# Kernel optimization log

Hardware: AMD Instinct MI355X
Metric: run time of the kernel (lower is better)

## Reference

```python
import jax, jax.numpy as jnp
import numpy as np
from jax import lax

CR = 16        # opt.cr (temporal dim)
HEADS = 4      # num_heads
DIM = 64       # dim == channel count c
B = 2          # true batch; input batch = B*CR
H = W = 128


def setup_inputs() -> dict:
    key = jax.random.key(0)
    k1, k2, k3, k4 = jax.random.split(key, 4)
    return {
        "x": jax.random.normal(k1, (B * CR, DIM, H, W), jnp.float32),
        "ln_weight": jnp.ones((DIM,), jnp.float32),
        "ln_bias": jnp.zeros((DIM,), jnp.float32),
        "qkv_w": jax.random.normal(k2, (3 * CR, CR), jnp.float32) * 0.05,   # 1x1 conv
        "dw_w": jax.random.normal(k3, (3 * CR, 1, 3, 3), jnp.float32) * 0.1,  # depthwise 3x3
        "proj_w": jax.random.normal(k4, (DIM, DIM), jnp.float32) * 0.05,   # 1x1 conv
        "temperature": jnp.ones((HEADS, 1, 1), jnp.float32),
    }


def reference(x, ln_weight, ln_bias, qkv_w, dw_w, proj_w, temperature):
    b, c, h, w = x.shape
    Bt = b // CR
    # WithBias LayerNorm over channel dim (per spatial location), eps=1e-5
    mu = jnp.mean(x, axis=1, keepdims=True)
    var = jnp.mean(jnp.square(x - mu), axis=1, keepdims=True)
    xn = (x - mu) / jnp.sqrt(var + 1e-5)
    xn = xn * ln_weight[None, :, None, None] + ln_bias[None, :, None, None]
    # (B*cr, c, h, w) -> (B, cr, c, h, w) -> (B*c, cr, h, w)
    x_in = xn.reshape(Bt, CR, c, h, w).transpose(0, 2, 1, 3, 4).reshape(Bt * c, CR, h, w)
    # 1x1 qkv conv (no bias)
    qkv = jnp.einsum('oc,bchw->bohw', qkv_w, x_in)
    # depthwise 3x3 conv, padding 1
    qkv = lax.conv_general_dilated(qkv, dw_w, (1, 1), 'SAME',
                                   feature_group_count=3 * CR,
                                   dimension_numbers=('NCHW', 'OIHW', 'NCHW'))
    q, k, v = jnp.split(qkv, 3, axis=1)
    ch = CR // HEADS  # per-head channel dim

    def heads(t):
        return t.reshape(Bt * c, HEADS, ch, h * w)

    def l2n(t):
        n = jnp.sqrt(jnp.sum(jnp.square(t), axis=-1, keepdims=True))
        return t / jnp.maximum(n, 1e-12)

    q, k, v = heads(q), heads(k), heads(v)
    q, k = l2n(q), l2n(k)
    # transposed (channel) attention: small ch x ch scores
    attn = jnp.einsum('bhcn,bhdn->bhcd', q, k) * temperature[None]
    attn = jax.nn.softmax(attn, axis=-1)
    out = jnp.einsum('bhcd,bhdn->bhcn', attn, v)  # (B*c, heads, ch, hw)
    # (B*c, cr, h, w) -> (B, c, cr, h, w) -> (B*cr, c, h, w)
    out = out.reshape(Bt * c, CR, h, w).reshape(Bt, c, CR, h, w)
    out = out.transpose(0, 2, 1, 3, 4).reshape(b, c, h, w)
    # 1x1 project_out
    return jnp.einsum('oc,bchw->bohw', proj_w, out)
```

## Files before the change

kernel.cpp:

```cpp
#include <hip/hip_runtime.h>
#include <hip/hip_fp16.h>

__device__ __forceinline__ float2 h2f2(unsigned int u) {
  return __half22float2(__builtin_bit_cast(__half2, u));
}
__device__ __forceinline__ unsigned int f2h2(float a, float b) {
  return __builtin_bit_cast(unsigned int, __floats2half2_rn(a, b));
}

#if __has_builtin(__builtin_amdgcn_fdot2)
typedef _Float16 h2v __attribute__((ext_vector_type(2)));
__device__ __forceinline__ float fdot2(unsigned int a, unsigned int b, float c) {
  return __builtin_amdgcn_fdot2(__builtin_bit_cast(h2v, a),
                                __builtin_bit_cast(h2v, b), c, false);
}
#else
__device__ __forceinline__ float fdot2(unsigned int a, unsigned int b, float c) {
  float2 fa = h2f2(a), fb = h2f2(b);
  return fmaf(fa.y, fb.y, fmaf(fa.x, fb.x, c));
}
#endif

__global__ __launch_bounds__(256) void k_stats(const float2* __restrict__ x2,
                                               float4* __restrict__ stats4) {
  int id = blockIdx.x * 256 + threadIdx.x;
  int bb = id >> 13;
  int jp = id & 8191;
  const float2* xp = x2 + ((size_t)bb << 19) + jp;
  float s0 = 0.f, q0 = 0.f, s1 = 0.f, q1 = 0.f;
#pragma unroll
  for (int ci = 0; ci < 64; ++ci) {
    float2 v = xp[(size_t)ci << 13];
    s0 += v.x; q0 = fmaf(v.x, v.x, q0);
    s1 += v.y; q1 = fmaf(v.y, v.y, q1);
  }
  float mu0 = s0 * (1.f / 64.f), mu1 = s1 * (1.f / 64.f);
  float4 r;
  r.x = mu0; r.y = rsqrtf(fmaf(-mu0, mu0, q0 * (1.f / 64.f)) + 1e-5f);
  r.z = mu1; r.w = rsqrtf(fmaf(-mu1, mu1, q1 * (1.f / 64.f)) + 1e-5f);
  stats4[id] = r;
}

__global__ __launch_bounds__(256) void k_wpack(
    const float* __restrict__ qkvw, const float* __restrict__ dww,
    const float* __restrict__ projw, unsigned int* __restrict__ qkvpk,
    unsigned int* __restrict__ dwpk, unsigned int* __restrict__ projpk) {
  int t = blockIdx.x * 256 + threadIdx.x;
  if (t < 2048) {
    int o = t >> 5, c2 = t & 31;
    projpk[t] = f2h2(projw[(o << 6) + 2 * c2], projw[(o << 6) + 2 * c2 + 1]);
  } else if (t < 2432) {
    int i = t - 2048;
    int ch = i >> 3, tp = i & 7;
    qkvpk[i] = f2h2(qkvw[(ch << 4) + 2 * tp], qkvw[(ch << 4) + 2 * tp + 1]);
  } else if (t < 2648) {
    int i = t - 2432;
    int pl = i / 9, k = i - pl * 9;
    dwpk[i] = f2h2(dww[18 * pl + k], dww[18 * pl + 9 + k]);
  }
}

__global__ __launch_bounds__(256) void k_fused(
    const float* __restrict__ x, const float2* __restrict__ stats2,
    const float* __restrict__ lnw, const float* __restrict__ lnb,
    const unsigned int* __restrict__ qkvpk, const unsigned int* __restrict__ dwpk,
    unsigned int* __restrict__ vbuf, float* __restrict__ Sacc,
    float* __restrict__ Nacc) {
  __shared__ unsigned int pre[2520];
  int tid = threadIdx.x;
  int bc = blockIdx.y, bt = bc >> 6, ci = bc & 63;
  int tx0 = (blockIdx.x & 3) << 5, ty0 = (blockIdx.x >> 2) << 4;
  float lw = lnw[ci], lb = lnb[ci];

  unsigned int wc[3][8];
  int waddr[3];
  {
    size_t xci = ((size_t)(bt * 1024 + ci)) << 14;
    int sbase = bt << 18;
#pragma unroll
    for (int it = 0; it < 3; ++it) {
      int pos = tid + (it << 8);
      bool act = pos < 612;
      int hy = pos / 34, hx = pos - hy * 34;
      int gy = ty0 + hy - 1, gx = tx0 + hx - 1;
      bool ok = act && ((unsigned)gy < 128u) && ((unsigned)gx < 128u);
      waddr[it] = act ? (hy * 35 + hx) : -1;
      int gp = (gy << 7) + gx;
#pragma unroll
      for (int tp = 0; tp < 8; ++tp) {
        unsigned int w = 0;
        if (ok) {
          float x0 = x[xci + ((size_t)(2 * tp) << 20) + gp];
          float x1 = x[xci + ((size_t)(2 * tp + 1) << 20) + gp];
          float2 s0 = stats2[sbase + (2 * tp) * 16384 + gp];
          float2 s1 = stats2[sbase + (2 * tp + 1) * 16384 + gp];
          w = f2h2(fmaf((x0 - s0.x) * s0.y, lw, lb),
                   fmaf((x1 - s1.x) * s1.y, lw, lb));
        }
        wc[it][tp] = w;
      }
    }
  }

  int iy = tid >> 4, jx = tid & 15;
  int dwbase = iy * 35 + 2 * jx;

  for (int h = 0; h < 4; ++h) {
#pragma unroll
    for (int it = 0; it < 3; ++it) {
      if (waddr[it] >= 0) {
        float acc[8];
#pragma unroll
        for (int c = 0; c < 8; ++c) {
          int gch = (c < 4) ? (4 * h + c) : (16 + 4 * h + (c - 4));
          float s = 0.f;
#pragma unroll
          for (int tp = 0; tp < 8; ++tp)
            s = fdot2(wc[it][tp], qkvpk[gch * 8 + tp], s);
          acc[c] = s;
        }
#pragma unroll
        for (int pl = 0; pl < 4; ++pl)
          pre[pl * 630 + waddr[it]] = f2h2(acc[2 * pl], acc[2 * pl + 1]);
      }
    }
    __syncthreads();
    unsigned int qkw[8];
#pragma unroll
    for (int pl = 0; pl < 4; ++pl) {
      int gpl = (pl < 2) ? (2 * h + pl) : (8 + 2 * h + (pl - 2));
      const unsigned int* wp = dwpk + gpl * 9;
      __half2 a0 = __floats2half2_rn(0.f, 0.f), a1 = a0;
      int base = pl * 630 + dwbase;
#pragma unroll
      for (int dy = 0; dy < 3; ++dy) {
        __half2 d0 = __builtin_bit_cast(__half2, pre[base + dy * 35 + 0]);
        __half2 d1 = __builtin_bit_cast(__half2, pre[base + dy * 35 + 1]);
        __half2 d2 = __builtin_bit_cast(__half2, pre[base + dy * 35 + 2]);
        __half2 d3 = __builtin_bit_cast(__half2, pre[base + dy * 35 + 3]);
        __half2 w0 = __builtin_bit_cast(__half2, wp[dy * 3 + 0]);
        __half2 w1 = __builtin_bit_cast(__half2, wp[dy * 3 + 1]);
        __half2 w2 = __builtin_bit_cast(__half2, wp[dy * 3 + 2]);
        a0 = __hfma2(w0, d0, a0); a0 = __hfma2(w1, d1, a0); a0 = __hfma2(w2, d2, a0);
        a1 = __hfma2(w0, d1, a1); a1 = __hfma2(w1, d2, a1); a1 = __hfma2(w2, d3, a1);
      }
      unsigned int u0 = __builtin_bit_cast(unsigned int, a0);
      unsigned int u1 = __builtin_bit_cast(unsigned int, a1);
      qkw[2 * pl]     = (u0 & 0xFFFFu) | (u1 << 16);
      qkw[2 * pl + 1] = (u0 >> 16) | (u1 & 0xFFFF0000u);
    }
    __syncthreads();
#pragma unroll
    for (int r = 0; r < 8; ++r) pre[r * 272 + tid] = qkw[r];
    __syncthreads();
    {
      int cd = tid >> 4, pc = tid & 15;
      int cc = cd >> 2, dd = cd & 3;
      const unsigned int* qrow = pre + cc * 272;
      const unsigned int* krow = pre + (4 + dd) * 272;
      float s = 0.f;
#pragma unroll
      for (int i = 0; i < 16; ++i)
        s = fdot2(qrow[pc + (i << 4)], krow[pc + (i << 4)], s);
      s += __shfl_xor(s, 1); s += __shfl_xor(s, 2);
      s += __shfl_xor(s, 4); s += __shfl_xor(s, 8);
      if (pc == 0) atomicAdd(&Sacc[((bc << 2) + h) * 16 + cc * 4 + dd], s);
    }
    {
      int row = tid >> 5, pc = tid & 31;
      const unsigned int* rp = pre + row * 272;
      float n = 0.f;
#pragma unroll
      for (int i = 0; i < 8; ++i) {
        unsigned int v = rp[pc + (i << 5)];
        n = fdot2(v, v, n);
      }
      n += __shfl_xor(n, 1); n += __shfl_xor(n, 2); n += __shfl_xor(n, 4);
      n += __shfl_xor(n, 8); n += __shfl_xor(n, 16);
      if (pc == 0) {
        int g = (row < 4) ? (4 * h + row) : (16 + 4 * h + (row - 4));
        atomicAdd(&Nacc[(bc << 5) + g], n);
      }
    }
    __syncthreads();
  }

  for (int vc = 0; vc < 2; ++vc) {
#pragma unroll
    for (int it = 0; it < 3; ++it) {
      if (waddr[it] >= 0) {
        float acc[8];
#pragma unroll
        for (int c = 0; c < 8; ++c) {
          int gch = 32 + 8 * vc + c;
          float s = 0.f;
#pragma unroll
          for (int tp = 0; tp < 8; ++tp)
            s = fdot2(wc[it][tp], qkvpk[gch * 8 + tp], s);
          acc[c] = s;
        }
#pragma unroll
        for (int pl = 0; pl < 4; ++pl)
          pre[pl * 630 + waddr[it]] = f2h2(acc[2 * pl], acc[2 * pl + 1]);
      }
    }
    __syncthreads();
#pragma unroll
    for (int pl = 0; pl < 4; ++pl) {
      int gpl = 16 + 4 * vc + pl;
      const unsigned int* wp = dwpk + gpl * 9;
      __half2 a0 = __floats2half2_rn(0.f, 0.f), a1 = a0;
      int base = pl * 630 + dwbase;
#pragma unroll
      for (int dy = 0; dy < 3; ++dy) {
        __half2 d0 = __builtin_bit_cast(__half2, pre[base + dy * 35 + 0]);
        __half2 d1 = __builtin_bit_cast(__half2, pre[base + dy * 35 + 1]);
        __half2 d2 = __builtin_bit_cast(__half2, pre[base + dy * 35 + 2]);
        __half2 d3 = __builtin_bit_cast(__half2, pre[base + dy * 35 + 3]);
        __half2 w0 = __builtin_bit_cast(__half2, wp[dy * 3 + 0]);
        __half2 w1 = __builtin_bit_cast(__half2, wp[dy * 3 + 1]);
        __half2 w2 = __builtin_bit_cast(__half2, wp[dy * 3 + 2]);
        a0 = __hfma2(w0, d0, a0); a0 = __hfma2(w1, d1, a0); a0 = __hfma2(w2, d2, a0);
        a1 = __hfma2(w0, d1, a1); a1 = __hfma2(w1, d2, a1); a1 = __hfma2(w2, d3, a1);
      }
      uint2 st2;
      st2.x = __builtin_bit_cast(unsigned int, a0);
      st2.y = __builtin_bit_cast(unsigned int, a1);
      size_t idx = ((size_t)(bc * 8 + 4 * vc + pl) << 14) +
                   (size_t)((ty0 + iy) << 7) + tx0 + 2 * jx;
      *reinterpret_cast<uint2*>(vbuf + idx) = st2;
    }
    __syncthreads();
  }
}

__global__ __launch_bounds__(256) void k_softmax(
    const float* __restrict__ Sacc, const float* __restrict__ Nacc,
    const float* __restrict__ temp, unsigned int* __restrict__ attnpk) {
  int idx = blockIdx.x * 256 + threadIdx.x;
  if (idx >= 512) return;
  int b = idx >> 2, hd = idx & 3;
  int bt = b >> 6, ci = b & 63;
  float tp = temp[hd];
  float iq[4], ik[4];
#pragma unroll
  for (int c = 0; c < 4; ++c) {
    iq[c] = 1.f / fmaxf(sqrtf(Nacc[(b << 5) + (hd << 2) + c]), 1e-12f);
    ik[c] = 1.f / fmaxf(sqrtf(Nacc[(b << 5) + 16 + (hd << 2) + c]), 1e-12f);
  }
  const float* Sp = Sacc + ((b << 2) + hd) * 16;
#pragma unroll
  for (int c = 0; c < 4; ++c) {
    float l[4];
#pragma unroll
    for (int d = 0; d < 4; ++d) l[d] = Sp[c * 4 + d] * iq[c] * ik[d] * tp;
    float m = fmaxf(fmaxf(l[0], l[1]), fmaxf(l[2], l[3]));
    float e0 = expf(l[0] - m), e1 = expf(l[1] - m);
    float e2 = expf(l[2] - m), e3 = expf(l[3] - m);
    float inv = 1.f / (e0 + e1 + e2 + e3);
    unsigned int* dst = attnpk + ((((bt * 4 + hd) * 4 + c) << 7) + ci * 2);
    dst[0] = f2h2(e0 * inv, e1 * inv);
    dst[1] = f2h2(e2 * inv, e3 * inv);
  }
}

__global__ __launch_bounds__(256) void k_outproj(
    const unsigned int* __restrict__ vbuf, const unsigned int* __restrict__ attnpk,
    const unsigned int* __restrict__ projpk, float* __restrict__ out) {
  int comb = blockIdx.y;
  int bt = comb >> 4, hd = (comb >> 2) & 3, c = comb & 3;
  int px = (blockIdx.x << 8) + threadIdx.x;

  const unsigned int* apk = attnpk + (((bt * 4 + hd) * 4 + c) << 7);
  float acc[64];
#pragma unroll
  for (int o = 0; o < 64; ++o) acc[o] = 0.f;

  size_t vbase = ((((size_t)bt * 512) + hd * 2) << 14) + px;
  for (int ci2 = 0; ci2 < 32; ++ci2) {
    size_t off0 = vbase + (((size_t)(2 * ci2) * 8) << 14);
    size_t off1 = off0 + ((size_t)8 << 14);
    unsigned int v0a = vbuf[off0];
    unsigned int v0b = vbuf[off0 + (1 << 14)];
    unsigned int v1a = vbuf[off1];
    unsigned int v1b = vbuf[off1 + (1 << 14)];
    float y0 = fdot2(v0a, apk[4 * ci2 + 0], fdot2(v0b, apk[4 * ci2 + 1], 0.f));
    float y1 = fdot2(v1a, apk[4 * ci2 + 2], fdot2(v1b, apk[4 * ci2 + 3], 0.f));
    unsigned int y2 = f2h2(y0, y1);
#pragma unroll
    for (int o = 0; o < 64; ++o)
      acc[o] = fdot2(y2, projpk[(o << 5) + ci2], acc[o]);
  }
  float* op = out + (((size_t)comb << 6) << 14) + px;
#pragma unroll
  for (int o = 0; o < 64; ++o) op[(size_t)o << 14] = acc[o];
}

extern "C" void kernel_launch(void* const* d_in, const int* in_sizes, int n_in,
                              void* d_out, int out_size, void* d_ws, size_t ws_size,
                              hipStream_t stream) {
  const float* x = (const float*)d_in[0];
  const float* lnw = (const float*)d_in[1];
  const float* lnb = (const float*)d_in[2];
  const float* qkvw = (const float*)d_in[3];
  const float* dww = (const float*)d_in[4];
  const float* projw = (const float*)d_in[5];
  const float* temp = (const float*)d_in[6];
  float* out = (float*)d_out;

  unsigned int* vbuf = (unsigned int*)d_ws;
  char* tail = (char*)d_ws + 67108864ull;
  float4* stats4 = (float4*)tail;
  float* Sacc = (float*)(tail + 4194304ull);
  float* Nacc = Sacc + 8192;
  unsigned int* attnpk = (unsigned int*)(Nacc + 4096);
  unsigned int* projpk = attnpk + 4096;
  unsigned int* qkvpk = projpk + 2048;
  unsigned int* dwpk = qkvpk + 384;

  hipMemsetAsync(Sacc, 0, (8192 + 4096) * sizeof(float), stream);
  k_stats<<<dim3(1024), dim3(256), 0, stream>>>((const float2*)x, stats4);
  k_wpack<<<dim3(11), dim3(256), 0, stream>>>(qkvw, dww, projw, qkvpk, dwpk, projpk);
  k_fused<<<dim3(32, 128), dim3(256), 0, stream>>>(
      x, (const float2*)stats4, lnw, lnb, qkvpk, dwpk, vbuf, Sacc, Nacc);
  k_softmax<<<dim3(2), dim3(256), 0, stream>>>(Sacc, Nacc, temp, attnpk);
  k_outproj<<<dim3(64, 32), dim3(256), 0, stream>>>(vbuf, attnpk, projpk, out);
}
```

Before: 207.2 us.

## Process two heads per pass in fused kernel and two pixels per thread in outproj

The fused kernel now handles two heads per iteration, and all eight V planes in one pass, using a doubled shared buffer. This halves the number of barrier-separated phases and atomic rounds. The output projection kernel now computes two adjacent pixels per thread with vectorized loads and stores, which reuses each projection weight load and halves the grid. The cost is more registers (128 accumulators in outproj, 16 packed values in fused) and double the LDS, which may reduce occupancy.

```diff
diff --git a/kernel.cpp b/kernel.cpp
--- a/kernel.cpp
+++ b/kernel.cpp
@@ -66,7 +66,7 @@
     const unsigned int* __restrict__ qkvpk, const unsigned int* __restrict__ dwpk,
     unsigned int* __restrict__ vbuf, float* __restrict__ Sacc,
     float* __restrict__ Nacc) {
-  __shared__ unsigned int pre[2520];
+  __shared__ unsigned int pre[5040];
   int tid = threadIdx.x;
   int bc = blockIdx.y, bt = bc >> 6, ci = bc & 63;
   int tx0 = (blockIdx.x & 3) << 5, ty0 = (blockIdx.x >> 2) << 4;
@@ -105,30 +105,29 @@
   int iy = tid >> 4, jx = tid & 15;
   int dwbase = iy * 35 + 2 * jx;
 
-  for (int h = 0; h < 4; ++h) {
+  for (int m = 0; m < 2; ++m) {
 #pragma unroll
     for (int it = 0; it < 3; ++it) {
       if (waddr[it] >= 0) {
-        float acc[8];
-#pragma unroll
-        for (int c = 0; c < 8; ++c) {
-          int gch = (c < 4) ? (4 * h + c) : (16 + 4 * h + (c - 4));
-          float s = 0.f;
-#pragma unroll
-          for (int tp = 0; tp < 8; ++tp)
-            s = fdot2(wc[it][tp], qkvpk[gch * 8 + tp], s);
-          acc[c] = s;
+#pragma unroll
+        for (int pl = 0; pl < 8; ++pl) {
+          int cE = 2 * pl;
+          int gchE = (cE < 8) ? (8 * m + cE) : (16 + 8 * m + (cE - 8));
+          float sE = 0.f, sO = 0.f;
+#pragma unroll
+          for (int tp = 0; tp < 8; ++tp) {
+            sE = fdot2(wc[it][tp], qkvpk[gchE * 8 + tp], sE);
+            sO = fdot2(wc[it][tp], qkvpk[(gchE + 1) * 8 + tp], sO);
+          }
+          pre[pl * 630 + waddr[it]] = f2h2(sE, sO);
         }
-#pragma unroll
-        for (int pl = 0; pl < 4; ++pl)
-          pre[pl * 630 + waddr[it]] = f2h2(acc[2 * pl], acc[2 * pl + 1]);
       }
     }
     __syncthreads();
-    unsigned int qkw[8];
-#pragma unroll
-    for (int pl = 0; pl < 4; ++pl) {
-      int gpl = (pl < 2) ? (2 * h + pl) : (8 + 2 * h + (pl - 2));
+    unsigned int qkw[16];
+#pragma unroll
+    for (int pl = 0; pl < 8; ++pl) {
+      int gpl = (pl < 4) ? (4 * m + pl) : (8 + 4 * m + (pl - 4));
       const unsigned int* wp = dwpk + gpl * 9;
       __half2 a0 = __floats2half2_rn(0.f, 0.f), a1 = a0;
       int base = pl * 630 + dwbase;
@@ -151,86 +150,80 @@
     }
     __syncthreads();
 #pragma unroll
-    for (int r = 0; r < 8; ++r) pre[r * 272 + tid] = qkw[r];
+    for (int r = 0; r < 16; ++r) pre[r * 272 + tid] = qkw[r];
     __syncthreads();
     {
-      int cd = tid >> 4, pc = tid & 15;
-      int cc = cd >> 2, dd = cd & 3;
-      const unsigned int* qrow = pre + cc * 272;
-      const unsigned int* krow = pre + (4 + dd) * 272;
+      int combo = tid >> 3, pc = tid & 7;
+      int hp = combo >> 4, cd = combo & 15, cc = cd >> 2, dd = cd & 3;
+      const unsigned int* qrow = pre + (4 * hp + cc) * 272;
+      const unsigned int* krow = pre + (8 + 4 * hp + dd) * 272;
       float s = 0.f;
 #pragma unroll
-      for (int i = 0; i < 16; ++i)
-        s = fdot2(qrow[pc + (i << 4)], krow[pc + (i << 4)], s);
-      s += __shfl_xor(s, 1); s += __shfl_xor(s, 2);
-      s += __shfl_xor(s, 4); s += __shfl_xor(s, 8);
-      if (pc == 0) atomicAdd(&Sacc[((bc << 2) + h) * 16 + cc * 4 + dd], s);
+      for (int i = 0; i < 32; ++i)
+        s = fdot2(qrow[pc + (i << 3)], krow[pc + (i << 3)], s);
+      s += __shfl_xor(s, 1); s += __shfl_xor(s, 2); s += __shfl_xor(s, 4);
+      if (pc == 0)
+        atomicAdd(&Sacc[((bc << 2) + 2 * m + hp) * 16 + cc * 4 + dd], s);
     }
     {
-      int row = tid >> 5, pc = tid & 31;
+      int row = tid >> 4, pc = tid & 15;
       const unsigned int* rp = pre + row * 272;
       float n = 0.f;
 #pragma unroll
-      for (int i = 0; i < 8; ++i) {
-        unsigned int v = rp[pc + (i << 5)];
+      for (int i = 0; i < 16; ++i) {
+        unsigned int v = rp[pc + (i << 4)];
         n = fdot2(v, v, n);
       }
-      n += __shfl_xor(n, 1); n += __shfl_xor(n, 2); n += __shfl_xor(n, 4);
-      n += __shfl_xor(n, 8); n += __shfl_xor(n, 16);
+      n += __shfl_xor(n, 1); n += __shfl_xor(n, 2);
+      n += __shfl_xor(n, 4); n += __shfl_xor(n, 8);
       if (pc == 0) {
-        int g = (row < 4) ? (4 * h + row) : (16 + 4 * h + (row - 4));
+        int g = (row < 8) ? (8 * m + row) : (16 + 8 * m + (row - 8));
         atomicAdd(&Nacc[(bc << 5) + g], n);
       }
     }
     __syncthreads();
   }
 
-  for (int vc = 0; vc < 2; ++vc) {
-#pragma unroll
-    for (int it = 0; it < 3; ++it) {
-      if (waddr[it] >= 0) {
-        float acc[8];
-#pragma unroll
-        for (int c = 0; c < 8; ++c) {
-          int gch = 32 + 8 * vc + c;
-          float s = 0.f;
-#pragma unroll
-          for (int tp = 0; tp < 8; ++tp)
-            s = fdot2(wc[it][tp], qkvpk[gch * 8 + tp], s);
-          acc[c] = s;
+#pragma unroll
+  for (int it = 0; it < 3; ++it) {
+    if (waddr[it] >= 0) {
+#pragma unroll
+      for (int pl = 0; pl < 8; ++pl) {
+        int gchE = 32 + 2 * pl;
+        float sE = 0.f, sO = 0.f;
+#pragma unroll
+        for (int tp = 0; tp < 8; ++tp) {
+          sE = fdot2(wc[it][tp], qkvpk[gchE * 8 + tp], sE);
+          sO = fdot2(wc[it][tp], qkvpk[(gchE + 1) * 8 + tp], sO);
         }
-#pragma unroll
-        for (int pl = 0; pl < 4; ++pl)
-          pre[pl * 630 + waddr[it]] = f2h2(acc[2 * pl], acc[2 * pl + 1]);
-      }
-    }
-    __syncthreads();
-#pragma unroll
-    for (int pl = 0; pl < 4; ++pl) {
-      int gpl = 16 + 4 * vc + pl;
-      const unsigned int* wp = dwpk + gpl * 9;
-      __half2 a0 = __floats2half2_rn(0.f, 0.f), a1 = a0;
-      int base = pl * 630 + dwbase;
-#pragma unroll
-      for (int dy = 0; dy < 3; ++dy) {
-        __half2 d0 = __builtin_bit_cast(__half2, pre[base + dy * 35 + 0]);
-        __half2 d1 = __builtin_bit_cast(__half2, pre[base + dy * 35 + 1]);
-        __half2 d2 = __builtin_bit_cast(__half2, pre[base + dy * 35 + 2]);
-        __half2 d3 = __builtin_bit_cast(__half2, pre[base + dy * 35 + 3]);
-        __half2 w0 = __builtin_bit_cast(__half2, wp[dy * 3 + 0]);
-        __half2 w1 = __builtin_bit_cast(__half2, wp[dy * 3 + 1]);
-        __half2 w2 = __builtin_bit_cast(__half2, wp[dy * 3 + 2]);
-        a0 = __hfma2(w0, d0, a0); a0 = __hfma2(w1, d1, a0); a0 = __hfma2(w2, d2, a0);
-        a1 = __hfma2(w0, d1, a1); a1 = __hfma2(w1, d2, a1); a1 = __hfma2(w2, d3, a1);
-      }
-      uint2 st2;
-      st2.x = __builtin_bit_cast(unsigned int, a0);
-      st2.y = __builtin_bit_cast(unsigned int, a1);
-      size_t idx = ((size_t)(bc * 8 + 4 * vc + pl) << 14) +
-                   (size_t)((ty0 + iy) << 7) + tx0 + 2 * jx;
-      *reinterpret_cast<uint2*>(vbuf + idx) = st2;
-    }
-    __syncthreads();
+        pre[pl * 630 + waddr[it]] = f2h2(sE, sO);
+      }
+    }
+  }
+  __syncthreads();
+#pragma unroll
+  for (int pl = 0; pl < 8; ++pl) {
+    const unsigned int* wp = dwpk + (16 + pl) * 9;
+    __half2 a0 = __floats2half2_rn(0.f, 0.f), a1 = a0;
+    int base = pl * 630 + dwbase;
+#pragma unroll
+    for (int dy = 0; dy < 3; ++dy) {
+      __half2 d0 = __builtin_bit_cast(__half2, pre[base + dy * 35 + 0]);
+      __half2 d1 = __builtin_bit_cast(__half2, pre[base + dy * 35 + 1]);
+      __half2 d2 = __builtin_bit_cast(__half2, pre[base + dy * 35 + 2]);
+      __half2 d3 = __builtin_bit_cast(__half2, pre[base + dy * 35 + 3]);
+      __half2 w0 = __builtin_bit_cast(__half2, wp[dy * 3 + 0]);
+      __half2 w1 = __builtin_bit_cast(__half2, wp[dy * 3 + 1]);
+      __half2 w2 = __builtin_bit_cast(__half2, wp[dy * 3 + 2]);
+      a0 = __hfma2(w0, d0, a0); a0 = __hfma2(w1, d1, a0); a0 = __hfma2(w2, d2, a0);
+      a1 = __hfma2(w0, d1, a1); a1 = __hfma2(w1, d2, a1); a1 = __hfma2(w2, d3, a1);
+    }
+    uint2 st2;
+    st2.x = __builtin_bit_cast(unsigned int, a0);
+    st2.y = __builtin_bit_cast(unsigned int, a1);
+    size_t idx = ((size_t)(bc * 8 + pl) << 14) +
+                 (size_t)((ty0 + iy) << 7) + tx0 + 2 * jx;
+    *reinterpret_cast<uint2*>(vbuf + idx) = st2;
   }
 }
 
@@ -269,31 +262,38 @@
     const unsigned int* __restrict__ projpk, float* __restrict__ out) {
   int comb = blockIdx.y;
   int bt = comb >> 4, hd = (comb >> 2) & 3, c = comb & 3;
-  int px = (blockIdx.x << 8) + threadIdx.x;
+  int px = ((blockIdx.x << 8) + threadIdx.x) << 1;
 
   const unsigned int* apk = attnpk + (((bt * 4 + hd) * 4 + c) << 7);
-  float acc[64];
-#pragma unroll
-  for (int o = 0; o < 64; ++o) acc[o] = 0.f;
+  float accA[64], accB[64];
+#pragma unroll
+  for (int o = 0; o < 64; ++o) { accA[o] = 0.f; accB[o] = 0.f; }
 
   size_t vbase = ((((size_t)bt * 512) + hd * 2) << 14) + px;
   for (int ci2 = 0; ci2 < 32; ++ci2) {
     size_t off0 = vbase + (((size_t)(2 * ci2) * 8) << 14);
     size_t off1 = off0 + ((size_t)8 << 14);
-    unsigned int v0a = vbuf[off0];
-    unsigned int v0b = vbuf[off0 + (1 << 14)];
-    unsigned int v1a = vbuf[off1];
-    unsigned int v1b = vbuf[off1 + (1 << 14)];
-    float y0 = fdot2(v0a, apk[4 * ci2 + 0], fdot2(v0b, apk[4 * ci2 + 1], 0.f));
-    float y1 = fdot2(v1a, apk[4 * ci2 + 2], fdot2(v1b, apk[4 * ci2 + 3], 0.f));
-    unsigned int y2 = f2h2(y0, y1);
-#pragma unroll
-    for (int o = 0; o < 64; ++o)
-      acc[o] = fdot2(y2, projpk[(o << 5) + ci2], acc[o]);
+    uint2 v0a = *reinterpret_cast<const uint2*>(&vbuf[off0]);
+    uint2 v0b = *reinterpret_cast<const uint2*>(&vbuf[off0 + (1 << 14)]);
+    uint2 v1a = *reinterpret_cast<const uint2*>(&vbuf[off1]);
+    uint2 v1b = *reinterpret_cast<const uint2*>(&vbuf[off1 + (1 << 14)]);
+    float y0A = fdot2(v0a.x, apk[4 * ci2 + 0], fdot2(v0b.x, apk[4 * ci2 + 1], 0.f));
+    float y0B = fdot2(v0a.y, apk[4 * ci2 + 0], fdot2(v0b.y, apk[4 * ci2 + 1], 0.f));
+    float y1A = fdot2(v1a.x, apk[4 * ci2 + 2], fdot2(v1b.x, apk[4 * ci2 + 3], 0.f));
+    float y1B = fdot2(v1a.y, apk[4 * ci2 + 2], fdot2(v1b.y, apk[4 * ci2 + 3], 0.f));
+    unsigned int y2A = f2h2(y0A, y1A);
+    unsigned int y2B = f2h2(y0B, y1B);
+#pragma unroll
+    for (int o = 0; o < 64; ++o) {
+      unsigned int w = projpk[(o << 5) + ci2];
+      accA[o] = fdot2(y2A, w, accA[o]);
+      accB[o] = fdot2(y2B, w, accB[o]);
+    }
   }
   float* op = out + (((size_t)comb << 6) << 14) + px;
 #pragma unroll
-  for (int o = 0; o < 64; ++o) op[(size_t)o << 14] = acc[o];
+  for (int o = 0; o < 64; ++o)
+    *reinterpret_cast<float2*>(&op[(size_t)o << 14]) = make_float2(accA[o], accB[o]);
 }
 
 extern "C" void kernel_launch(void* const* d_in, const int* in_sizes, int n_in,
@@ -324,5 +324,5 @@
   k_fused<<<dim3(32, 128), dim3(256), 0, stream>>>(
       x, (const float2*)stats4, lnw, lnb, qkvpk, dwpk, vbuf, Sacc, Nacc);
   k_softmax<<<dim3(2), dim3(256), 0, stream>>>(Sacc, Nacc, temp, attnpk);
-  k_outproj<<<dim3(64, 32), dim3(256), 0, stream>>>(vbuf, attnpk, projpk, out);
-}
+  k_outproj<<<dim3(32, 32), dim3(256), 0, stream>>>(vbuf, attnpk, projpk, out);
+}
```

Result: no change. 207.3 us (+0.0%).
